# Kernel tuning notes

Measured on AMD Instinct MI355X. Metric: run time of the kernel, lower is better.

## Reference

```python
import jax, jax.numpy as jnp
import numpy as np

B, N, M = 16, 4096, 1024
C_IN, C_SKIP, C_OUT = 256, 128, 256
K = 3
BN_EPS = 1e-5


def setup_inputs() -> dict:
    key = jax.random.key(0)
    ks = jax.random.split(key, 6)
    s1 = (6.0 / (C_IN + C_SKIP + C_OUT)) ** 0.5  # xavier-uniform bound, ~scale
    s2 = (6.0 / (2 * C_OUT)) ** 0.5
    return {
        "points": jax.random.normal(ks[0], (B, 3, N), jnp.float32),
        "point_features": jax.random.normal(ks[1], (B, C_SKIP, N), jnp.float32),
        "centroids": jax.random.normal(ks[2], (B, 3, M), jnp.float32),
        "centroid_features": jax.random.normal(ks[3], (B, C_IN, M), jnp.float32),
        "W1": jax.random.uniform(ks[4], (C_OUT, C_IN + C_SKIP), jnp.float32, -s1, s1),
        "b1": jnp.zeros((C_OUT,), jnp.float32),
        "gamma": jnp.ones((C_OUT,), jnp.float32),
        "beta": jnp.zeros((C_OUT,), jnp.float32),
        "W2": jax.random.uniform(ks[5], (C_OUT, C_OUT), jnp.float32, -s2, s2),
        "b2": jnp.zeros((C_OUT,), jnp.float32),
    }


def _knn_interpolate(x, pos_x, pos_y):
    # x: [B,M,C], pos_x: [B,M,3], pos_y: [B,N,3]. torch_geometric knn_interpolate, k=3.
    d2 = (jnp.sum(pos_y * pos_y, -1)[:, :, None]
          + jnp.sum(pos_x * pos_x, -1)[:, None, :]
          - 2.0 * jnp.einsum('bnd,bmd->bnm', pos_y, pos_x))  # [B,N,M]
    neg_vals, idx = jax.lax.top_k(-d2, K)                    # k smallest distances
    w = 1.0 / jnp.maximum(-neg_vals, 1e-16)                  # inverse-squared-distance weights
    # original computes indices/weights under torch.no_grad()
    idx = jax.lax.stop_gradient(idx)
    w = jax.lax.stop_gradient(w)
    xk = jax.vmap(lambda xb, ib: xb[ib])(x, idx)             # [B,N,K,C]
    return jnp.einsum('bnkc,bnk->bnc', xk, w) / jnp.sum(w, -1, keepdims=True)


def reference(points, point_features, centroids, centroid_features,
              W1, b1, gamma, beta, W2, b2):
    # Faithful to the original torch .reshape/.view calls on channel-first layout
    pos_y = points.reshape(-1, 3).reshape(B, N, 3)
    pos_x = centroids.reshape(-1, 3).reshape(B, M, 3)
    x = centroid_features.reshape(-1, C_IN).reshape(B, M, C_IN)
    interp = _knn_interpolate(x, pos_x, pos_y)               # [B,N,C_IN]
    interp = interp.reshape(-1, C_IN).reshape(B, C_IN, N)    # faithful .view(B, C, -1)
    h = jnp.concatenate([point_features, interp], axis=1)    # [B, C_SKIP+C_IN, N]
    # Conv1d(kernel=1) -> channel GEMM
    h = jnp.einsum('oc,bcn->bon', W1, h) + b1[None, :, None]
    # BatchNorm1d, training mode (biased batch var), eps=1e-5
    mean = jnp.mean(h, axis=(0, 2), keepdims=True)
    var = jnp.var(h, axis=(0, 2), keepdims=True)
    h = (h - mean) * jax.lax.rsqrt(var + BN_EPS) * gamma[None, :, None] + beta[None, :, None]
    h = jax.nn.relu(h)
    return jnp.einsum('oc,bcn->bon', W2, h) + b2[None, :, None]
```

## Files before the change

kernel.cpp:

```cpp
#include <hip/hip_runtime.h>

#define BB   16
#define NN   4096
#define MM   1024
#define CIN  256
#define CSK  128
#define COUT 256
#define KCH  384
#define NP   65536
#define NSEG2 512
#define NCHUNK 8
#define MCH  (MM / NCHUNK)
#define CVB  32

typedef __attribute__((ext_vector_type(8))) short bf16x8;
typedef __attribute__((ext_vector_type(4))) float f32x4;
typedef __attribute__((ext_vector_type(8))) unsigned short ushort8v;
typedef __attribute__((ext_vector_type(4))) unsigned short ushort4v;

static __device__ __forceinline__ unsigned short f2bf(float f) {
    unsigned u = __builtin_bit_cast(unsigned, f);
    u += 0x7fffu + ((u >> 16) & 1u);
    return (unsigned short)(u >> 16);
}
static __device__ __forceinline__ float bf2f(unsigned short h) {
    unsigned u = ((unsigned)h) << 16;
    return __builtin_bit_cast(float, u);
}

__global__ __launch_bounds__(256) void megak_kernel(
    const float* __restrict__ pts, const float* __restrict__ cen,
    float* __restrict__ pdist, int* __restrict__ pidx,
    const float* __restrict__ cf, unsigned short* __restrict__ cfb,
    const float* __restrict__ pf, unsigned short* __restrict__ HbT,
    const float* __restrict__ W1, const float* __restrict__ W2,
    unsigned short* __restrict__ W1b, unsigned short* __restrict__ W2b)
{
    __shared__ union { float4 sc[MCH]; float ls[64][65]; } su;
    int blk = blockIdx.x;
    int t = threadIdx.x;

    if (blk < 2048) {
        int p0    = (blk >> 3) * 256;
        int chunk = blk & 7;
        int b     = p0 >> 12;
        int m0    = chunk * MCH;
        const float* cb = cen + (size_t)b * 3 * MM + 3 * m0;
        if (t < MCH) {
            float x = cb[3*t], y = cb[3*t+1], z = cb[3*t+2];
            su.sc[t] = make_float4(x, y, z, x*x + y*y + z*z);
        }
        __syncthreads();

        int p = p0 + t;
        int n = p & (NN - 1);
        const float* pb = pts + (size_t)b * 3 * NN;
        float px = pb[3*n], py = pb[3*n+1], pz = pb[3*n+2];
        float pw = px*px + py*py + pz*pz;

        float d0 = 1e30f, d1 = 1e30f, d2v = 1e30f;
        int   i0 = 0, i1 = 0, i2 = 0;
        #pragma unroll 16
        for (int m = 0; m < MCH; ++m) {
            float4 c = su.sc[m];
            float dot = px*c.x + py*c.y + pz*c.z;
            float d = (pw + c.w) - 2.0f * dot;
            bool c0 = d < d0, c1 = d < d1, c2 = d < d2v;
            int ni2 = c1 ? i1 : (c2 ? m : i2);
            int ni1 = c0 ? i0 : (c1 ? m : i1);
            int ni0 = c0 ? m  : i0;
            float nd1 = __builtin_amdgcn_fmed3f(d, d0, d1);
            float nd2 = __builtin_amdgcn_fmed3f(d, d1, d2v);
            d0 = fminf(d0, d);
            d1 = nd1; d2v = nd2;
            i0 = ni0; i1 = ni1; i2 = ni2;
        }
        int base = (p * NCHUNK + chunk) * 3;
        pdist[base] = d0;      pdist[base+1] = d1;      pdist[base+2] = d2v;
        pidx[base]  = m0 + i0; pidx[base+1]  = m0 + i1; pidx[base+2]  = m0 + i2;
        return;
    }
    if (blk < 4096) {
        int g = blk - 2048;
        size_t e8 = ((size_t)g * 256 + t) * 8;
        const float4* cf4 = (const float4*)(cf + e8);
        float4 a = cf4[0], b4 = cf4[1];
        ushort8v w;
        w[0]=f2bf(a.x); w[1]=f2bf(a.y); w[2]=f2bf(a.z); w[3]=f2bf(a.w);
        w[4]=f2bf(b4.x); w[5]=f2bf(b4.y); w[6]=f2bf(b4.z); w[7]=f2bf(b4.w);
        *(ushort8v*)&cfb[e8] = w;
        return;
    }
    if (blk < 6144) {
        int g = blk - 4096;
        int b = g >> 7;
        int r = g & 127;
        int n0 = (r >> 1) * 64;
        int c0 = (r & 1) * 64;
        const float* src = pf + (size_t)b * CSK * NN;
        #pragma unroll
        for (int i = 0; i < 16; ++i) {
            int id = t + i * 256;
            int cc = id >> 6, nn = id & 63;
            su.ls[nn][cc] = src[(size_t)(c0 + cc) * NN + n0 + nn];
        }
        __syncthreads();
        int row = t & 63, ch0 = (t >> 6) * 16;
        unsigned short* dst = HbT + ((size_t)b * NN + n0 + row) * KCH + c0 + ch0;
        #pragma unroll
        for (int g2 = 0; g2 < 2; ++g2) {
            ushort8v w;
            #pragma unroll
            for (int j = 0; j < 8; ++j) w[j] = f2bf(su.ls[row][ch0 + g2*8 + j]);
            *(ushort8v*)&dst[g2*8] = w;
        }
        return;
    }
    {
        int i = (blk - 6144) * 256 + t;
        if (i < COUT * KCH) W1b[i] = f2bf(W1[i]);
        else {
            int j = i - COUT * KCH;
            if (j < COUT * COUT) W2b[j] = f2bf(W2[j]);
        }
    }
}

__global__ __launch_bounds__(256) void interp_kernel(
    const unsigned short* __restrict__ cfb, const float* __restrict__ pdist,
    const int* __restrict__ pidx, unsigned short* __restrict__ HbT)
{
    __shared__ int   li[CVB][3];
    __shared__ float lw[CVB][3];
    __shared__ unsigned short tile[CVB][258];
    int xcd = blockIdx.x & 7;
    int j   = blockIdx.x >> 3;
    int b   = xcd * 2 + (j >> 7);
    int rem = j & 127;
    int hi  = rem >> 3;
    int ch  = rem & 7;
    int t = threadIdx.x;
    if (t < CVB) {
        int P = b * NN + (ch * CVB + t) * 16 + hi;
        float d0 = 1e30f, d1 = 1e30f, d2v = 1e30f;
        int   i0 = 0, i1 = 0, i2 = 0;
        int base = P * NCHUNK * 3;
        #pragma unroll
        for (int c = 0; c < NCHUNK * 3; ++c) {
            float d = pdist[base + c];
            int   i = pidx[base + c];
            bool c2 = d < d2v, c1 = d < d1, c0 = d < d0;
            d2v = c1 ? d1 : (c2 ? d : d2v);
            i2  = c1 ? i1 : (c2 ? i : i2);
            d1  = c0 ? d0 : (c1 ? d : d1);
            i1  = c0 ? i0 : (c1 ? i : i1);
            d0  = c0 ? d  : d0;
            i0  = c0 ? i  : i0;
        }
        float w0 = 1.0f / fmaxf(d0,  1e-16f);
        float w1 = 1.0f / fmaxf(d1,  1e-16f);
        float w2 = 1.0f / fmaxf(d2v, 1e-16f);
        float inv = 1.0f / (w0 + w1 + w2);
        li[t][0] = i0;     li[t][1] = i1;     li[t][2] = i2;
        lw[t][0] = w0*inv; lw[t][1] = w1*inv; lw[t][2] = w2*inv;
    }
    __syncthreads();
    const unsigned short* cfbb = cfb + (size_t)b * MM * CIN;
    #pragma unroll 4
    for (int cv = 0; cv < CVB; ++cv) {
        float v = lw[cv][0] * bf2f(cfbb[(size_t)li[cv][0] * CIN + t])
                + lw[cv][1] * bf2f(cfbb[(size_t)li[cv][1] * CIN + t])
                + lw[cv][2] * bf2f(cfbb[(size_t)li[cv][2] * CIN + t]);
        tile[cv][t] = f2bf(v);
    }
    __syncthreads();
    size_t dstbase = ((size_t)b * NN + hi * 256 + t) * KCH + CSK + ch * CVB;
    #pragma unroll
    for (int g = 0; g < CVB / 8; ++g) {
        ushort8v w;
        #pragma unroll
        for (int j2 = 0; j2 < 8; ++j2) w[j2] = tile[g*8 + j2][t];
        *(ushort8v*)&HbT[dstbase + g*8] = w;
    }
}

__global__ __launch_bounds__(256) void gemm1_kernel(
    const unsigned short* __restrict__ HbT, const unsigned short* __restrict__ W1b,
    const float* __restrict__ b1, unsigned short* __restrict__ h1T,
    float* __restrict__ psum, float* __restrict__ psq)
{
    __shared__ union {
        struct {
            __align__(16) unsigned short As[128][40];
            __align__(16) unsigned short Bs[128][40];
        } s;
        struct {
            __align__(16) unsigned short eps[64][136];
            float red[512];
        } e;
    } u;
    int pp0 = blockIdx.x * 128;
    int o0  = blockIdx.y * 128;
    int t = threadIdx.x;
    int wid = t >> 6, lane = t & 63;
    int wr = wid >> 1, wc = wid & 1;
    int lr = lane & 15, lk = lane >> 4;

    int rowi[2], qi[2];
    ushort8v ra[2], rb[2];
    #pragma unroll
    for (int i = 0; i < 2; ++i) { int id = t + i*256; rowi[i] = id >> 2; qi[i] = id & 3; }
    #pragma unroll
    for (int i = 0; i < 2; ++i) {
        ra[i] = *(const ushort8v*)&W1b[(size_t)(o0 + rowi[i]) * KCH + qi[i]*8];
        rb[i] = *(const ushort8v*)&HbT[(size_t)(pp0 + rowi[i]) * KCH + qi[i]*8];
    }

    f32x4 acc[4][4] = {};

    for (int c0 = 0; c0 < KCH; c0 += 32) {
        #pragma unroll
        for (int i = 0; i < 2; ++i) {
            *(ushort8v*)&u.s.As[rowi[i]][qi[i]*8] = ra[i];
            *(ushort8v*)&u.s.Bs[rowi[i]][qi[i]*8] = rb[i];
        }
        __syncthreads();
        int cn = (c0 + 32 < KCH) ? c0 + 32 : c0;
        #pragma unroll
        for (int i = 0; i < 2; ++i) {
            ra[i] = *(const ushort8v*)&W1b[(size_t)(o0 + rowi[i]) * KCH + cn + qi[i]*8];
            rb[i] = *(const ushort8v*)&HbT[(size_t)(pp0 + rowi[i]) * KCH + cn + qi[i]*8];
        }
        bf16x8 af[4], bfr[4];
        #pragma unroll
        for (int m = 0; m < 4; ++m) af[m] = *(const bf16x8*)&u.s.As[wr*64 + m*16 + lr][lk*8];
        #pragma unroll
        for (int n = 0; n < 4; ++n) bfr[n] = *(const bf16x8*)&u.s.Bs[wc*64 + n*16 + lr][lk*8];
        #pragma unroll
        for (int m = 0; m < 4; ++m)
            #pragma unroll
            for (int n = 0; n < 4; ++n)
                acc[m][n] = __builtin_amdgcn_mfma_f32_16x16x32_bf16(af[m], bfr[n], acc[m][n], 0, 0, 0);
        __syncthreads();
    }
    float bb[4][4];
    #pragma unroll
    for (int m = 0; m < 4; ++m)
        #pragma unroll
        for (int j = 0; j < 4; ++j)
            bb[m][j] = b1[o0 + wr*64 + m*16 + lk*4 + j];
    float sprt[4][4] = {{0.f}}, qprt[4][4] = {{0.f}};
    #pragma unroll
    for (int pw = 0; pw < 2; ++pw) {
        if (wc == pw) {
            #pragma unroll
            for (int n = 0; n < 4; ++n) {
                int r = n*16 + lr;
                #pragma unroll
                for (int m = 0; m < 4; ++m) {
                    f32x4 v = acc[m][n];
                    ushort4v w;
                    #pragma unroll
                    for (int j = 0; j < 4; ++j) {
                        float f = v[j] + bb[m][j];
                        w[j] = f2bf(f);
                        float rr = bf2f(w[j]);
                        sprt[m][j] += rr;
                        qprt[m][j] = fmaf(rr, rr, qprt[m][j]);
                    }
                    *(ushort4v*)&u.e.eps[r][wr*64 + m*16 + lk*4] = w;
                }
            }
        }
        __syncthreads();
        {
            int r = t >> 2, seg = t & 3;
            size_t gbase = ((size_t)(pp0 + pw*64 + r)) * COUT + o0 + seg * 32;
            #pragma unroll
            for (int k = 0; k < 4; ++k) {
                ushort8v vv = *(const ushort8v*)&u.e.eps[r][seg*32 + k*8];
                *(ushort8v*)&h1T[gbase + k*8] = vv;
            }
        }
        __syncthreads();
    }
    #pragma unroll
    for (int m = 0; m < 4; ++m)
        #pragma unroll
        for (int j = 0; j < 4; ++j) {
            float s = sprt[m][j], q = qprt[m][j];
            #pragma unroll
            for (int off = 1; off < 16; off <<= 1) {
                s += __shfl_xor(s, off, 64);
                q += __shfl_xor(q, off, 64);
            }
            sprt[m][j] = s; qprt[m][j] = q;
        }
    if (lr == 0) {
        #pragma unroll
        for (int m = 0; m < 4; ++m)
            #pragma unroll
            for (int j = 0; j < 4; ++j) {
                int ol = wr*64 + m*16 + lk*4 + j;
                u.e.red[wc*128 + ol]       = sprt[m][j];
                u.e.red[256 + wc*128 + ol] = qprt[m][j];
            }
    }
    __syncthreads();
    if (t < 128) {
        float S = u.e.red[t] + u.e.red[128 + t];
        float Q = u.e.red[256 + t] + u.e.red[384 + t];
        psum[(size_t)(o0 + t) * NSEG2 + blockIdx.x] = S;
        psq [(size_t)(o0 + t) * NSEG2 + blockIdx.x] = Q;
    }
}

__global__ __launch_bounds__(256) void bnfin_kernel(
    const float* __restrict__ psum, const float* __restrict__ psq,
    const float* __restrict__ gamma, const float* __restrict__ beta,
    float* __restrict__ bnscale, float* __restrict__ bnshift)
{
    __shared__ float rs[256], rq[256];
    int o = blockIdx.x, t = threadIdx.x;
    rs[t] = psum[(size_t)o * NSEG2 + t] + psum[(size_t)o * NSEG2 + 256 + t];
    rq[t] = psq [(size_t)o * NSEG2 + t] + psq [(size_t)o * NSEG2 + 256 + t];
    __syncthreads();
    for (int off = 128; off > 0; off >>= 1) {
        if (t < off) { rs[t] += rs[t + off]; rq[t] += rq[t + off]; }
        __syncthreads();
    }
    if (t == 0) {
        float mean = rs[0] * (1.0f / NP);
        float var  = rq[0] * (1.0f / NP) - mean * mean;
        float sc = gamma[o] * rsqrtf(var + 1e-5f);
        bnscale[o] = sc;
        bnshift[o] = fmaf(-mean, sc, beta[o]);
    }
}

__global__ __launch_bounds__(256) void gemm2_kernel(
    const unsigned short* __restrict__ h1T, const unsigned short* __restrict__ W2b,
    const float* __restrict__ b2, const float* __restrict__ bnscale,
    const float* __restrict__ bnshift, float* __restrict__ out)
{
    __shared__ union {
        struct {
            __align__(16) unsigned short As[128][40];
            __align__(16) unsigned short Bs[128][40];
        } s;
        float eps[64][132];
    } u;
    __shared__ float scs[COUT], shs[COUT];
    int pp0 = blockIdx.x * 128;
    int o0  = blockIdx.y * 128;
    int t = threadIdx.x;
    scs[t] = bnscale[t]; shs[t] = bnshift[t];
    int wid = t >> 6, lane = t & 63;
    int wr = wid >> 1, wc = wid & 1;
    int lr = lane & 15, lk = lane >> 4;

    int rowi[2], qi[2];
    ushort8v ra[2], rb[2];
    #pragma unroll
    for (int i = 0; i < 2; ++i) { int id = t + i*256; rowi[i] = id >> 2; qi[i] = id & 3; }
    #pragma unroll
    for (int i = 0; i < 2; ++i) {
        ra[i] = *(const ushort8v*)&W2b[(size_t)(o0 + rowi[i]) * COUT + qi[i]*8];
        rb[i] = *(const ushort8v*)&h1T[(size_t)(pp0 + rowi[i]) * COUT + qi[i]*8];
    }
    f32x4 acc[4][4] = {};
    __syncthreads();

    for (int c0 = 0; c0 < COUT; c0 += 32) {
        #pragma unroll
        for (int i = 0; i < 2; ++i) {
            *(ushort8v*)&u.s.As[rowi[i]][qi[i]*8] = ra[i];
            ushort8v bv;
            #pragma unroll
            for (int j = 0; j < 8; ++j) {
                float f = fmaf(bf2f(rb[i][j]), scs[c0 + qi[i]*8 + j], shs[c0 + qi[i]*8 + j]);
                bv[j] = f2bf(fmaxf(f, 0.0f));
            }
            *(ushort8v*)&u.s.Bs[rowi[i]][qi[i]*8] = bv;
        }
        __syncthreads();
        int cn = (c0 + 32 < COUT) ? c0 + 32 : c0;
        #pragma unroll
        for (int i = 0; i < 2; ++i) {
            ra[i] = *(const ushort8v*)&W2b[(size_t)(o0 + rowi[i]) * COUT + cn + qi[i]*8];
            rb[i] = *(const ushort8v*)&h1T[(size_t)(pp0 + rowi[i]) * COUT + cn + qi[i]*8];
        }
        bf16x8 af[4], bfr[4];
        #pragma unroll
        for (int m = 0; m < 4; ++m) af[m] = *(const bf16x8*)&u.s.As[wr*64 + m*16 + lr][lk*8];
        #pragma unroll
        for (int n = 0; n < 4; ++n) bfr[n] = *(const bf16x8*)&u.s.Bs[wc*64 + n*16 + lr][lk*8];
        #pragma unroll
        for (int m = 0; m < 4; ++m)
            #pragma unroll
            for (int n = 0; n < 4; ++n)
                acc[m][n] = __builtin_amdgcn_mfma_f32_16x16x32_bf16(af[m], bfr[n], acc[m][n], 0, 0, 0);
        __syncthreads();
    }
    int b  = pp0 >> 12;
    int n0 = pp0 & (NN - 1);
    float b2v[4][4];
    #pragma unroll
    for (int m = 0; m < 4; ++m)
        #pragma unroll
        for (int j = 0; j < 4; ++j)
            b2v[m][j] = b2[o0 + wr*64 + m*16 + lk*4 + j];
    #pragma unroll
    for (int ow = 0; ow < 2; ++ow) {
        if (wr == ow) {
            #pragma unroll
            for (int m = 0; m < 4; ++m)
                #pragma unroll
                for (int n = 0; n < 4; ++n) {
                    f32x4 v = acc[m][n];
                    int pl = wc*64 + n*16 + lr;
                    #pragma unroll
                    for (int j = 0; j < 4; ++j)
                        u.eps[m*16 + lk*4 + j][pl] = v[j] + b2v[m][j];
                }
        }
        __syncthreads();
        #pragma unroll
        for (int i = 0; i < 8; ++i) {
            int r  = (t >> 5) + i * 8;
            int c4 = (t & 31) * 4;
            float4 v = *(const float4*)&u.eps[r][c4];
            *(float4*)&out[((size_t)(b * COUT + o0 + ow*64 + r)) * NN + n0 + c4] = v;
        }
        __syncthreads();
    }
}

extern "C" void kernel_launch(void* const* d_in, const int* in_sizes, int n_in,
                              void* d_out, int out_size, void* d_ws, size_t ws_size,
                              hipStream_t stream)
{
    const float* pts   = (const float*)d_in[0];
    const float* pf    = (const float*)d_in[1];
    const float* cen   = (const float*)d_in[2];
    const float* cf    = (const float*)d_in[3];
    const float* W1    = (const float*)d_in[4];
    const float* b1    = (const float*)d_in[5];
    const float* gamma = (const float*)d_in[6];
    const float* beta  = (const float*)d_in[7];
    const float* W2    = (const float*)d_in[8];
    const float* b2    = (const float*)d_in[9];
    float* out = (float*)d_out;

    char* ws = (char*)d_ws;
    size_t off = 0;
    unsigned short* HbT = (unsigned short*)(ws + off); off += (size_t)NP * KCH * 2;
    unsigned short* h1T = (unsigned short*)(ws + off); off += (size_t)NP * COUT * 2;
    unsigned short* W1b = (unsigned short*)(ws + off); off += (size_t)COUT * KCH * 2;
    unsigned short* W2b = (unsigned short*)(ws + off); off += (size_t)COUT * COUT * 2;
    unsigned short* cfb = (unsigned short*)(ws + off); off += (size_t)BB * MM * CIN * 2;
    float* pdist   = (float*)(ws + off); off += (size_t)NP * NCHUNK * 3 * sizeof(float);
    int*   pidx    = (int*)(ws + off);   off += (size_t)NP * NCHUNK * 3 * sizeof(int);
    float* psum    = (float*)(ws + off); off += (size_t)COUT * NSEG2 * sizeof(float);
    float* psq     = (float*)(ws + off); off += (size_t)COUT * NSEG2 * sizeof(float);
    float* bnscale = (float*)(ws + off); off += 1024;
    float* bnshift = (float*)(ws + off); off += 1024;
    (void)ws_size; (void)in_sizes; (void)n_in; (void)out_size;

    hipLaunchKernelGGL(megak_kernel,  dim3(6784),         dim3(256), 0, stream,
                       pts, cen, pdist, pidx, cf, cfb, pf, HbT, W1, W2, W1b, W2b);
    hipLaunchKernelGGL(interp_kernel, dim3(2048),         dim3(256), 0, stream,
                       cfb, pdist, pidx, HbT);
    hipLaunchKernelGGL(gemm1_kernel,  dim3(NP / 128, 2),  dim3(256), 0, stream,
                       HbT, W1b, b1, h1T, psum, psq);
    hipLaunchKernelGGL(bnfin_kernel,  dim3(COUT),         dim3(256), 0, stream,
                       psum, psq, gamma, beta, bnscale, bnshift);
    hipLaunchKernelGGL(gemm2_kernel,  dim3(NP / 128, 2),  dim3(256), 0, stream,
                       h1T, W2b, b2, bnscale, bnshift, out);
}
```

Before: 134.2 us.

## Use direct global-to-LDS double-buffered loads in gemm1 and inline-asm KNN selection

The gemm1 main loop now uses global_load_lds to fetch A and B tiles straight into double-buffered, XOR-swizzled LDS. This replaces register staging plus explicit LDS stores and drops one barrier per k-step. Separately, the KNN top-3 insertion is written as hand-written compare/cndmask/med3 inline assembly, with the unroll reduced from 16 to 8, to tighten the per-centroid instruction count. Risks: the inline asm limits compiler scheduling, and the async LDS loads rely on correct waitcnt ordering before the barrier.

After: 135.8 us. About the same (+1.2%).

```diff
diff --git a/kernel.cpp b/kernel.cpp
--- a/kernel.cpp
+++ b/kernel.cpp
@@ -28,6 +28,25 @@
     return __builtin_bit_cast(float, u);
 }
 
+#define KSEL(d, m) do {                                                     \
+    unsigned long long cc0, cc1, cc2;                                       \
+    asm("v_cmp_lt_f32 %[c0], %[vd], %[vd0]\n\t"                             \
+        "v_cmp_lt_f32 %[c1], %[vd], %[vd1]\n\t"                             \
+        "v_cmp_lt_f32 %[c2], %[vd], %[vd2]\n\t"                             \
+        "v_cndmask_b32 %[vi2], %[vi2], %[vm], %[c2]\n\t"                    \
+        "v_cndmask_b32 %[vi2], %[vi2], %[vi1], %[c1]\n\t"                   \
+        "v_cndmask_b32 %[vi1], %[vi1], %[vm], %[c1]\n\t"                    \
+        "v_cndmask_b32 %[vi1], %[vi1], %[vi0], %[c0]\n\t"                   \
+        "v_cndmask_b32 %[vi0], %[vi0], %[vm], %[c0]\n\t"                    \
+        "v_med3_f32 %[vd2], %[vd], %[vd1], %[vd2]\n\t"                      \
+        "v_med3_f32 %[vd1], %[vd], %[vd0], %[vd1]\n\t"                      \
+        "v_min_f32 %[vd0], %[vd0], %[vd]"                                   \
+        : [vd0]"+v"(d0), [vd1]"+v"(d1), [vd2]"+v"(d2v),                     \
+          [vi0]"+v"(i0), [vi1]"+v"(i1), [vi2]"+v"(i2),                      \
+          [c0]"=&s"(cc0), [c1]"=&s"(cc1), [c2]"=&s"(cc2)                    \
+        : [vd]"v"(d), [vm]"v"(m));                                          \
+} while (0)
+
 __global__ __launch_bounds__(256) void megak_kernel(
     const float* __restrict__ pts, const float* __restrict__ cen,
     float* __restrict__ pdist, int* __restrict__ pidx,
@@ -60,20 +79,12 @@
 
         float d0 = 1e30f, d1 = 1e30f, d2v = 1e30f;
         int   i0 = 0, i1 = 0, i2 = 0;
-        #pragma unroll 16
+        #pragma unroll 8
         for (int m = 0; m < MCH; ++m) {
             float4 c = su.sc[m];
             float dot = px*c.x + py*c.y + pz*c.z;
             float d = (pw + c.w) - 2.0f * dot;
-            bool c0 = d < d0, c1 = d < d1, c2 = d < d2v;
-            int ni2 = c1 ? i1 : (c2 ? m : i2);
-            int ni1 = c0 ? i0 : (c1 ? m : i1);
-            int ni0 = c0 ? m  : i0;
-            float nd1 = __builtin_amdgcn_fmed3f(d, d0, d1);
-            float nd2 = __builtin_amdgcn_fmed3f(d, d1, d2v);
-            d0 = fminf(d0, d);
-            d1 = nd1; d2v = nd2;
-            i0 = ni0; i1 = ni1; i2 = ni2;
+            KSEL(d, m);
         }
         int base = (p * NCHUNK + chunk) * 3;
         pdist[base] = d0;      pdist[base+1] = d1;      pdist[base+2] = d2v;
@@ -184,6 +195,11 @@
     }
 }
 
+#define SWZ(r) (((r) >> 1) & 3)
+#define GLL(g, l) __builtin_amdgcn_global_load_lds(                          \
+    (const __attribute__((address_space(1))) unsigned int*)(g),              \
+    (__attribute__((address_space(3))) unsigned int*)(l), 16, 0, 0)
+
 __global__ __launch_bounds__(256) void gemm1_kernel(
     const unsigned short* __restrict__ HbT, const unsigned short* __restrict__ W1b,
     const float* __restrict__ b1, unsigned short* __restrict__ h1T,
@@ -191,8 +207,8 @@
 {
     __shared__ union {
         struct {
-            __align__(16) unsigned short As[128][40];
-            __align__(16) unsigned short Bs[128][40];
+            __align__(16) unsigned short A[2][128 * 32];
+            __align__(16) unsigned short B[2][128 * 32];
         } s;
         struct {
             __align__(16) unsigned short eps[64][136];
@@ -202,40 +218,56 @@
     int pp0 = blockIdx.x * 128;
     int o0  = blockIdx.y * 128;
     int t = threadIdx.x;
-    int wid = t >> 6, lane = t & 63;
-    int wr = wid >> 1, wc = wid & 1;
-    int lr = lane & 15, lk = lane >> 4;
-
-    int rowi[2], qi[2];
-    ushort8v ra[2], rb[2];
-    #pragma unroll
-    for (int i = 0; i < 2; ++i) { int id = t + i*256; rowi[i] = id >> 2; qi[i] = id & 3; }
-    #pragma unroll
-    for (int i = 0; i < 2; ++i) {
-        ra[i] = *(const ushort8v*)&W1b[(size_t)(o0 + rowi[i]) * KCH + qi[i]*8];
-        rb[i] = *(const ushort8v*)&HbT[(size_t)(pp0 + rowi[i]) * KCH + qi[i]*8];
+    int wv = t >> 6, L = t & 63;
+    int wr = wv >> 1, wc = wv & 1;
+    int lr = L & 15, lk = L >> 4;
+
+    const unsigned short* gA[2];
+    const unsigned short* gB[2];
+    int ldso[2];
+    #pragma unroll
+    for (int j = 0; j < 2; ++j) {
+        int row = wv*32 + j*16 + (L >> 2);
+        int sg  = (L & 3) ^ SWZ(row);
+        gA[j] = W1b + (size_t)(o0 + row) * KCH + sg*8;
+        gB[j] = HbT + (size_t)(pp0 + row) * KCH + sg*8;
+        ldso[j] = wv*1024 + j*512;
+    }
+    int offA[4], offB[4];
+    #pragma unroll
+    for (int m = 0; m < 4; ++m) {
+        int ar = wr*64 + m*16 + lr;
+        offA[m] = ar*32 + (lk ^ SWZ(ar))*8;
+    }
+    #pragma unroll
+    for (int n = 0; n < 4; ++n) {
+        int br = wc*64 + n*16 + lr;
+        offB[n] = br*32 + (lk ^ SWZ(br))*8;
     }
 
     f32x4 acc[4][4] = {};
 
-    for (int c0 = 0; c0 < KCH; c0 += 32) {
-        #pragma unroll
-        for (int i = 0; i < 2; ++i) {
-            *(ushort8v*)&u.s.As[rowi[i]][qi[i]*8] = ra[i];
-            *(ushort8v*)&u.s.Bs[rowi[i]][qi[i]*8] = rb[i];
-        }
-        __syncthreads();
-        int cn = (c0 + 32 < KCH) ? c0 + 32 : c0;
-        #pragma unroll
-        for (int i = 0; i < 2; ++i) {
-            ra[i] = *(const ushort8v*)&W1b[(size_t)(o0 + rowi[i]) * KCH + cn + qi[i]*8];
-            rb[i] = *(const ushort8v*)&HbT[(size_t)(pp0 + rowi[i]) * KCH + cn + qi[i]*8];
+    #pragma unroll
+    for (int j = 0; j < 2; ++j) {
+        GLL(gA[j], &u.s.A[0][ldso[j]]);
+        GLL(gB[j], &u.s.B[0][ldso[j]]);
+    }
+    __syncthreads();
+
+    for (int ks = 0; ks < KCH / 32; ++ks) {
+        int cur = ks & 1;
+        if (ks + 1 < KCH / 32) {
+            #pragma unroll
+            for (int j = 0; j < 2; ++j) {
+                GLL(gA[j] + (ks + 1) * 32, &u.s.A[cur ^ 1][ldso[j]]);
+                GLL(gB[j] + (ks + 1) * 32, &u.s.B[cur ^ 1][ldso[j]]);
+            }
         }
         bf16x8 af[4], bfr[4];
         #pragma unroll
-        for (int m = 0; m < 4; ++m) af[m] = *(const bf16x8*)&u.s.As[wr*64 + m*16 + lr][lk*8];
-        #pragma unroll
-        for (int n = 0; n < 4; ++n) bfr[n] = *(const bf16x8*)&u.s.Bs[wc*64 + n*16 + lr][lk*8];
+        for (int m = 0; m < 4; ++m) af[m] = *(const bf16x8*)&u.s.A[cur][offA[m]];
+        #pragma unroll
+        for (int n = 0; n < 4; ++n) bfr[n] = *(const bf16x8*)&u.s.B[cur][offB[n]];
         #pragma unroll
         for (int m = 0; m < 4; ++m)
             #pragma unroll
@@ -243,6 +275,7 @@
                 acc[m][n] = __builtin_amdgcn_mfma_f32_16x16x32_bf16(af[m], bfr[n], acc[m][n], 0, 0, 0);
         __syncthreads();
     }
+
     float bb[4][4];
     #pragma unroll
     for (int m = 0; m < 4; ++m)
```
